# Optimization experiments

Measured on AMD Instinct MI355X. Metric: run time of the kernel, lower is better.

## Reference

```python
import jax, jax.numpy as jnp
from jax import lax
import numpy as np

B, S, V, H = 128, 1024, 128, 256


def setup_inputs() -> dict:
    key = jax.random.key(0)
    ks = jax.random.split(key, 12)
    sc = 1.0 / np.sqrt(H)
    return {
        "x": jax.random.normal(ks[0], (B, S, V), jnp.float32),
        "W_ih0": jax.random.normal(ks[1], (4 * H, V), jnp.float32) * sc,
        "W_hh0": jax.random.normal(ks[2], (4 * H, H), jnp.float32) * sc,
        "b_ih0": jax.random.normal(ks[3], (4 * H,), jnp.float32) * sc,
        "b_hh0": jax.random.normal(ks[4], (4 * H,), jnp.float32) * sc,
        "W_ih1": jax.random.normal(ks[5], (4 * H, H), jnp.float32) * sc,
        "W_hh1": jax.random.normal(ks[6], (4 * H, H), jnp.float32) * sc,
        "b_ih1": jax.random.normal(ks[7], (4 * H,), jnp.float32) * sc,
        "b_hh1": jax.random.normal(ks[8], (4 * H,), jnp.float32) * sc,
        "W_out": jax.random.normal(ks[9], (V, H), jnp.float32) * sc,
        "b_out": jax.random.normal(ks[10], (V,), jnp.float32) * sc,
    }


def _lstm_layer(x, W_ih, W_hh, b_ih, b_hh):
    # x: [B, S, in]; PyTorch gate order i, f, g, o along the 4H axis.
    b, s, _ = x.shape
    h_dim = W_hh.shape[1]
    # Precompute input contributions for all timesteps (one big GEMM).
    xg = jnp.einsum('bsi,gi->bsg', x, W_ih) + b_ih + b_hh  # [B, S, 4H]

    def step(carry, xg_t):
        h, c = carry
        g = xg_t + h @ W_hh.T  # [B, 4H]
        i, f, gg, o = jnp.split(g, 4, axis=-1)
        c = jax.nn.sigmoid(f) * c + jax.nn.sigmoid(i) * jnp.tanh(gg)
        h = jax.nn.sigmoid(o) * jnp.tanh(c)
        return (h, c), h

    h0 = jnp.zeros((b, h_dim), x.dtype)
    (_, _), hs = lax.scan(step, (h0, h0), jnp.swapaxes(xg, 0, 1))  # hs: [S, B, H]
    return jnp.swapaxes(hs, 0, 1)


def reference(x, W_ih0, W_hh0, b_ih0, b_hh0, W_ih1, W_hh1, b_ih1, b_hh1, W_out, b_out):
    h1 = _lstm_layer(x, W_ih0, W_hh0, b_ih0, b_hh0)
    h2 = _lstm_layer(h1, W_ih1, W_hh1, b_ih1, b_hh1)
    return jnp.einsum('bsh,vh->bsv', h2, W_out) + b_out
```

## Files before the change

kernel.cpp:

```cpp
#include <hip/hip_runtime.h>
#include <cstdint>

#define NB 128
#define NS 1024
#define NV 128
#define NH 256
#define CH 64
#define NCH (NS / CH)

typedef _Float16 f16;
typedef _Float16 h2 __attribute__((ext_vector_type(2)));
typedef _Float16 f16x8 __attribute__((ext_vector_type(8)));
typedef float f32x4 __attribute__((ext_vector_type(4)));
typedef uint32_t u32;

static __device__ __forceinline__ float fdot2(u32 a, u32 b, float c) {
  return __builtin_amdgcn_fdot2(__builtin_bit_cast(h2, a),
                                __builtin_bit_cast(h2, b), c, false);
}
static __device__ __forceinline__ u32 pkh(float a, float b) {
  union { h2 h; u32 u; } cv; cv.h = h2{(f16)a, (f16)b}; return cv.u;
}
static __device__ __forceinline__ u32 pkz(float a, float b) {
  return __builtin_bit_cast(u32, __builtin_amdgcn_cvt_pkrtz(a, b));
}
static __device__ __forceinline__ float sigm(float x) { return 1.f / (1.f + __expf(-x)); }
static __device__ __forceinline__ float tanh_(float x) { return 1.f - 2.f / (__expf(2.f * x) + 1.f); }

static __device__ __forceinline__ void pin4v(uint4& v) {
  asm volatile("" : "+v"(v.x), "+v"(v.y), "+v"(v.z), "+v"(v.w));
}

__global__ __launch_bounds__(1024) void prepack_kernel(
    const float* __restrict__ Wih0, const float* __restrict__ Wih1,
    const float* __restrict__ Whh0, const float* __restrict__ Whh1,
    u32* __restrict__ Wih0p, u32* __restrict__ Wih1p,
    u32* __restrict__ Whh0p, u32* __restrict__ Whh1p) {
  const int g = blockIdx.x * 1024 + threadIdx.x;
  const float* src; u32* dst; int off;
  if (g < 65536)       { src = Wih0; dst = Wih0p; off = g; }
  else if (g < 196608) { src = Wih1; dst = Wih1p; off = g - 65536; }
  else if (g < 327680) { src = Whh0; dst = Whh0p; off = g - 196608; }
  else                 { src = Whh1; dst = Whh1p; off = g - 327680; }
  dst[off] = pkh(src[2 * off], src[2 * off + 1]);
}

#define P1S 132
#define P0S 68
__global__ __launch_bounds__(512) void gemm_pair_kernel(
    const u32* __restrict__ g1_in, const u32* __restrict__ g1_Wp,
    const float* __restrict__ g1_bih, const float* __restrict__ g1_bhh,
    f16* __restrict__ g1_xg, int g1_t0, int g1_on,
    const float* __restrict__ g0_x, const u32* __restrict__ g0_Wp,
    const float* __restrict__ g0_bih, const float* __restrict__ g0_bhh,
    f16* __restrict__ g0_xg, int g0_t0, int g0_on) {
  __shared__ __align__(16) u32 panel[64 * P1S];
  const int tid = threadIdx.x;
  const int blk = blockIdx.x;
  const int lane = tid & 63;
  const int w = tid >> 6;
  const int lrow = lane & 15;
  const int lk = lane >> 4;

  if (blk < 128) {
    if (!g1_on) return;
    const int b = blk;
    {
      const uint4* src = (const uint4*)(g1_in + ((size_t)b * NS + g1_t0) * 128);
      const int t = tid >> 3, cc = tid & 7;
#pragma unroll
      for (int q = 0; q < 4; ++q) {
        uint4 v = src[t * 32 + cc * 4 + q];
        *(uint4*)&panel[t * P1S + cc * 16 + q * 4] = v;
      }
    }
    float bs[8];
#pragma unroll
    for (int n = 0; n < 8; ++n) {
      const int r = w * 128 + n * 16 + lrow;
      bs[n] = g1_bih[r] + g1_bhh[r];
    }
    __syncthreads();
    f32x4 acc[4][8] = {};
#pragma unroll 1
    for (int kc = 0; kc < 8; ++kc) {
      uint4 af[4];
#pragma unroll
      for (int m = 0; m < 4; ++m)
        af[m] = *(const uint4*)&panel[(m * 16 + lrow) * P1S + kc * 16 + lk * 4];
#pragma unroll
      for (int n = 0; n < 8; ++n) {
        const int r = w * 128 + n * 16 + lrow;
        uint4 bf = *(const uint4*)(g1_Wp + (size_t)r * 128 + kc * 16 + lk * 4);
#pragma unroll
        for (int m = 0; m < 4; ++m)
          acc[m][n] = __builtin_amdgcn_mfma_f32_16x16x32_f16(
              __builtin_bit_cast(f16x8, af[m]), __builtin_bit_cast(f16x8, bf),
              acc[m][n], 0, 0, 0);
      }
    }
#pragma unroll
    for (int m = 0; m < 4; ++m)
#pragma unroll
      for (int n = 0; n < 8; ++n) {
        const int r = w * 128 + n * 16 + lrow;
#pragma unroll
        for (int j = 0; j < 4; ++j) {
          const int t = m * 16 + lk * 4 + j;
          g1_xg[((size_t)b * CH + t) * 1024 + r] = (f16)(acc[m][n][j] + bs[n]);
        }
      }
  } else {
    if (!g0_on) return;
    const int b = blk - 128;
    {
      const float4* src = (const float4*)(g0_x + ((size_t)b * NS + g0_t0) * NV);
      const int t = tid >> 3, cc = tid & 7;
      float4 v0 = src[t * 32 + cc * 4 + 0];
      float4 v1 = src[t * 32 + cc * 4 + 1];
      float4 v2 = src[t * 32 + cc * 4 + 2];
      float4 v3 = src[t * 32 + cc * 4 + 3];
      *(uint4*)&panel[t * P0S + cc * 8 + 0] =
          uint4{pkz(v0.x, v0.y), pkz(v0.z, v0.w), pkz(v1.x, v1.y), pkz(v1.z, v1.w)};
      *(uint4*)&panel[t * P0S + cc * 8 + 4] =
          uint4{pkz(v2.x, v2.y), pkz(v2.z, v2.w), pkz(v3.x, v3.y), pkz(v3.z, v3.w)};
    }
    float bs[8];
#pragma unroll
    for (int n = 0; n < 8; ++n) {
      const int r = w * 128 + n * 16 + lrow;
      bs[n] = g0_bih[r] + g0_bhh[r];
    }
    __syncthreads();
    f32x4 acc[4][8] = {};
#pragma unroll 1
    for (int kc = 0; kc < 4; ++kc) {
      uint4 af[4];
#pragma unroll
      for (int m = 0; m < 4; ++m)
        af[m] = *(const uint4*)&panel[(m * 16 + lrow) * P0S + kc * 16 + lk * 4];
#pragma unroll
      for (int n = 0; n < 8; ++n) {
        const int r = w * 128 + n * 16 + lrow;
        uint4 bf = *(const uint4*)(g0_Wp + (size_t)r * 64 + kc * 16 + lk * 4);
#pragma unroll
        for (int m = 0; m < 4; ++m)
          acc[m][n] = __builtin_amdgcn_mfma_f32_16x16x32_f16(
              __builtin_bit_cast(f16x8, af[m]), __builtin_bit_cast(f16x8, bf),
              acc[m][n], 0, 0, 0);
      }
    }
#pragma unroll
    for (int m = 0; m < 4; ++m)
#pragma unroll
      for (int n = 0; n < 8; ++n) {
        const int r = w * 128 + n * 16 + lrow;
#pragma unroll
        for (int j = 0; j < 4; ++j) {
          const int t = m * 16 + lk * 4 + j;
          g0_xg[((size_t)b * CH + t) * 1024 + r] = (f16)(acc[m][n][j] + bs[n]);
        }
      }
  }
}

__global__ __attribute__((amdgpu_flat_work_group_size(1024, 1024),
                          amdgpu_waves_per_eu(4, 4)))
void scan_pair_kernel(
    const f16* __restrict__ xgA, const u32* __restrict__ WhhAp,
    u32* __restrict__ slotsA, u32* __restrict__ hseedA, float* __restrict__ carryA,
    int t0A, int firstA, int onA,
    const f16* __restrict__ xgB, const u32* __restrict__ WhhBp,
    u32* __restrict__ slotsB, u32* __restrict__ hseedB, float* __restrict__ carryB,
    int t0B, int firstB, int onB) {
  __shared__ uint4 wL0[4][1024];
  __shared__ uint4 wL1[4][1024];
  __shared__ __align__(16) u32 hbuf[2][128];

  const int blk = blockIdx.x;
  const int tid = threadIdx.x;
  const f16* xg; const u32* Whhp; u32* slots; u32* hseed; float* carry;
  int t0, first, b;
  if (blk < 128) {
    if (!onA) return;
    b = blk; xg = xgA; Whhp = WhhAp; slots = slotsA; hseed = hseedA; carry = carryA;
    t0 = t0A; first = firstA;
  } else {
    if (!onB) return;
    b = blk - 128; xg = xgB; Whhp = WhhBp; slots = slotsB; hseed = hseedB; carry = carryB;
    t0 = t0B; first = firstB;
  }
  const int kh = tid & 1;
  const int gp = (tid >> 1) & 1;
  const int u = tid >> 2;
  const int r0 = gp * 256 + u;
  const int r1 = r0 + 512;

  uint4 w0v[12], w1v[12];
  {
    const u32* p0 = Whhp + (size_t)r0 * 128 + kh * 64;
    const u32* p1 = Whhp + (size_t)r1 * 128 + kh * 64;
#pragma unroll
    for (int k = 0; k < 16; ++k) {
      uint4 v0 = *(const uint4*)(p0 + 4 * k);
      uint4 v1 = *(const uint4*)(p1 + 4 * k);
      if (k < 12) { w0v[k] = v0; w1v[k] = v1; }
      else { wL0[k - 12][tid] = v0; wL1[k - 12][tid] = v1; }
    }
  }
#pragma unroll
  for (int k = 0; k < 12; ++k) { pin4v(w0v[k]); pin4v(w1v[k]); }
  float c;
  if (first) {
    if (tid < 128) hbuf[0][tid] = 0u;
    c = 0.f;
  } else {
    if (tid < 128) hbuf[0][tid] = hseed[b * 128 + tid];
    c = carry[b * 256 + u];
  }
  __syncthreads();

#pragma unroll 1
  for (int tl = 0; tl < CH; ++tl) {
    const int cur = tl & 1, nxt = cur ^ 1;
    const f16* xp = xg + ((size_t)b * CH + tl) * 1024;
    const float xa = (float)xp[r0];
    const float xb = (float)xp[r1];

    float a0 = 0.f, a1 = 0.f;
#pragma unroll
    for (int k = 0; k < 16; ++k) {
      uint4 hk = *(const uint4*)&hbuf[cur][kh * 64 + 4 * k];
      const uint4 wa = (k < 12) ? w0v[k] : wL0[k - 12][tid];
      const uint4 wb = (k < 12) ? w1v[k] : wL1[k - 12][tid];
      a0 = fdot2(wa.x, hk.x, a0); a0 = fdot2(wa.y, hk.y, a0);
      a0 = fdot2(wa.z, hk.z, a0); a0 = fdot2(wa.w, hk.w, a0);
      a1 = fdot2(wb.x, hk.x, a1); a1 = fdot2(wb.y, hk.y, a1);
      a1 = fdot2(wb.z, hk.z, a1); a1 = fdot2(wb.w, hk.w, a1);
    }
    a0 += __shfl_xor(a0, 1);
    a1 += __shfl_xor(a1, 1);
    a0 += xa; a1 += xb;
    const float px0 = __shfl_xor(a0, 2);
    const float px1 = __shfl_xor(a1, 2);
    const float gi = sigm(gp ? px0 : a0);
    const float gf = sigm(gp ? a0 : px0);
    const float gg = tanh_(gp ? px1 : a1);
    const float go = sigm(gp ? a1 : px1);
    c = gf * c + gi * gg;
    const float h = go * tanh_(c);
    if ((tid & 3) == 0) {
      ((f16*)hbuf[nxt])[u] = (f16)h;
      ((f16*)(slots + ((size_t)b * NS + t0 + tl) * 128))[u] = (f16)h;
    }
    __syncthreads();
  }
  if (tid < 128) hseed[b * 128 + tid] = hbuf[0][tid];
  if ((tid & 3) == 0) carry[b * 256 + u] = c;
}

#define OPS 140
static __device__ __forceinline__ int swzc(int col) { return col + 4 * (col >> 5); }

__global__ __launch_bounds__(1024) void outproj_kernel(
    const float* __restrict__ Wout, const float* __restrict__ bout,
    u32* __restrict__ io) {
  const int bs = blockIdx.x;
  const int b = bs >> 4;
  const int t0 = (bs & 15) * 64;
  const int tid = threadIdx.x;
  const int p = tid & 7;
  const int vq = tid >> 3;

  __shared__ u32 h1L[64 * OPS];
  __shared__ float outL[64 * OPS];

  const u32* src = io + ((size_t)b * NS + t0) * 128;
  uint4 s0 = *(const uint4*)(src + (size_t)tid * 8);
  uint4 s1 = *(const uint4*)(src + (size_t)tid * 8 + 4);

  u32 wo[16];
  const float* pw = Wout + (size_t)vq * NH + p * 32;
#pragma unroll
  for (int k = 0; k < 8; ++k) {
    float4 w4 = *(const float4*)(pw + 4 * k);
    wo[2 * k] = pkh(w4.x, w4.y); wo[2 * k + 1] = pkh(w4.z, w4.w);
  }
  const float bo = bout[vq];

  {
    const int sr = tid >> 4;
    const int sc = (tid & 15) * 8;
    const int base = sr * OPS + swzc(sc);
    *(uint4*)&h1L[base] = s0;
    *(uint4*)&h1L[base + 4] = s1;
  }
  __syncthreads();

#pragma unroll 4
  for (int s = 0; s < 64; ++s) {
    float oa = 0.f;
#pragma unroll
    for (int q = 0; q < 4; ++q) {
      uint4 hq = *(const uint4*)&h1L[s * OPS + swzc(p * 16 + 4 * q)];
      u32 hw[4] = {hq.x, hq.y, hq.z, hq.w};
#pragma unroll
      for (int j = 0; j < 4; ++j) oa = fdot2(wo[4 * q + j], hw[j], oa);
    }
    oa += __shfl_xor(oa, 1);
    oa += __shfl_xor(oa, 2);
    oa += __shfl_xor(oa, 4);
    if (p == 0) outL[s * OPS + swzc(vq)] = oa + bo;
  }
  __syncthreads();

  float* df = (float*)(io + ((size_t)b * NS + t0) * 128);
  {
    const int sr = tid >> 4;
    const int sc = (tid & 15) * 8;
    const int base = sr * OPS + swzc(sc);
    *(float4*)(df + (size_t)tid * 8) = *(float4*)&outL[base];
    *(float4*)(df + (size_t)tid * 8 + 4) = *(float4*)&outL[base + 4];
  }
}

extern "C" void kernel_launch(void* const* d_in, const int* in_sizes, int n_in,
                              void* d_out, int out_size, void* d_ws, size_t ws_size,
                              hipStream_t stream) {
  const float* x    = (const float*)d_in[0];
  const float* Wih0 = (const float*)d_in[1];
  const float* Whh0 = (const float*)d_in[2];
  const float* bih0 = (const float*)d_in[3];
  const float* bhh0 = (const float*)d_in[4];
  const float* Wih1 = (const float*)d_in[5];
  const float* Whh1 = (const float*)d_in[6];
  const float* bih1 = (const float*)d_in[7];
  const float* bhh1 = (const float*)d_in[8];
  const float* Wout = (const float*)d_in[9];
  const float* bout = (const float*)d_in[10];

  f16* xg0 = (f16*)d_ws;
  f16* xg1 = (f16*)((char*)d_ws + (16u << 20));
  u32* hseed0 = (u32*)((char*)d_ws + (32u << 20));
  u32* hseed1 = (u32*)((char*)d_ws + (32u << 20) + (64u << 10));
  float* carry0 = (float*)((char*)d_ws + (32u << 20) + (128u << 10));
  float* carry1 = (float*)((char*)d_ws + (32u << 20) + (256u << 10));
  u32* Wih0p = (u32*)((char*)d_ws + (34u << 20));
  u32* Wih1p = (u32*)((char*)d_ws + (35u << 20));
  u32* Whh0p = (u32*)((char*)d_ws + (36u << 20));
  u32* Whh1p = (u32*)((char*)d_ws + (37u << 20));
  u32* slots = (u32*)d_out;

  prepack_kernel<<<448, 1024, 0, stream>>>(Wih0, Wih1, Whh0, Whh1,
                                           Wih0p, Wih1p, Whh0p, Whh1p);

  gemm_pair_kernel<<<256, 512, 0, stream>>>(
      nullptr, nullptr, nullptr, nullptr, nullptr, 0, 0,
      x, Wih0p, bih0, bhh0, xg0, 0, 1);
  scan_pair_kernel<<<256, 1024, 0, stream>>>(
      nullptr, nullptr, nullptr, nullptr, nullptr, 0, 0, 0,
      xg0, Whh0p, slots, hseed0, carry0, 0, 1, 1);

  for (int s = 0; s < NCH; ++s) {
    const int g0on = (s + 1 < NCH);
    gemm_pair_kernel<<<256, 512, 0, stream>>>(
        slots, Wih1p, bih1, bhh1, xg1, s * CH, 1,
        x, Wih0p, bih0, bhh0, xg0, (s + 1) * CH, g0on);
    scan_pair_kernel<<<256, 1024, 0, stream>>>(
        xg1, Whh1p, slots, hseed1, carry1, s * CH, (s == 0) ? 1 : 0, 1,
        xg0, Whh0p, slots, hseed0, carry0, (s + 1) * CH, 0, g0on);
  }
  outproj_kernel<<<2048, 1024, 0, stream>>>(Wout, bout, slots);
}
```

Before: 3.492 ms.

## Halve scan block to 512 threads with full-K rows per thread and readlane broadcast

The recurrent scan kernel drops from 1024 to 512 threads per block. Each thread now owns the whole K=256 reduction for two gate rows, so the cross-lane shuffle that combined K halves goes away. More of W_hh is kept in registers (24 of 32 uint4 chunks per row), with the remainder in LDS. The second half of the hidden vector is broadcast with readlane from a per-lane register copy instead of LDS reads, which cuts LDS traffic. The cost is twice the serial dot-product work per thread, much higher register pressure, and fewer waves to hide latency.

```diff
diff --git a/kernel.cpp b/kernel.cpp
--- a/kernel.cpp
+++ b/kernel.cpp
@@ -164,8 +164,8 @@
   }
 }
 
-__global__ __attribute__((amdgpu_flat_work_group_size(1024, 1024),
-                          amdgpu_waves_per_eu(4, 4)))
+__global__ __attribute__((amdgpu_flat_work_group_size(512, 512),
+                          amdgpu_waves_per_eu(2, 2)))
 void scan_pair_kernel(
     const f16* __restrict__ xgA, const u32* __restrict__ WhhAp,
     u32* __restrict__ slotsA, u32* __restrict__ hseedA, float* __restrict__ carryA,
@@ -173,8 +173,8 @@
     const f16* __restrict__ xgB, const u32* __restrict__ WhhBp,
     u32* __restrict__ slotsB, u32* __restrict__ hseedB, float* __restrict__ carryB,
     int t0B, int firstB, int onB) {
-  __shared__ uint4 wL0[4][1024];
-  __shared__ uint4 wL1[4][1024];
+  __shared__ uint4 wL0[8][512];
+  __shared__ uint4 wL1[8][512];
   __shared__ __align__(16) u32 hbuf[2][128];
 
   const int blk = blockIdx.x;
@@ -190,26 +190,26 @@
     b = blk - 128; xg = xgB; Whhp = WhhBp; slots = slotsB; hseed = hseedB; carry = carryB;
     t0 = t0B; first = firstB;
   }
-  const int kh = tid & 1;
-  const int gp = (tid >> 1) & 1;
-  const int u = tid >> 2;
-  const int r0 = gp * 256 + u;
+  const int p = tid & 1;
+  const int u = tid >> 1;
+  const int lane = tid & 63;
+  const int r0 = p * 256 + u;
   const int r1 = r0 + 512;
 
-  uint4 w0v[12], w1v[12];
+  uint4 w0r[24], w1r[24];
   {
-    const u32* p0 = Whhp + (size_t)r0 * 128 + kh * 64;
-    const u32* p1 = Whhp + (size_t)r1 * 128 + kh * 64;
-#pragma unroll
-    for (int k = 0; k < 16; ++k) {
+    const u32* p0 = Whhp + (size_t)r0 * 128;
+    const u32* p1 = Whhp + (size_t)r1 * 128;
+#pragma unroll
+    for (int k = 0; k < 32; ++k) {
       uint4 v0 = *(const uint4*)(p0 + 4 * k);
       uint4 v1 = *(const uint4*)(p1 + 4 * k);
-      if (k < 12) { w0v[k] = v0; w1v[k] = v1; }
-      else { wL0[k - 12][tid] = v0; wL1[k - 12][tid] = v1; }
-    }
-  }
-#pragma unroll
-  for (int k = 0; k < 12; ++k) { pin4v(w0v[k]); pin4v(w1v[k]); }
+      if (k < 24) { w0r[k] = v0; w1r[k] = v1; }
+      else { wL0[k - 24][tid] = v0; wL1[k - 24][tid] = v1; }
+    }
+  }
+#pragma unroll
+  for (int k = 0; k < 24; ++k) { pin4v(w0r[k]); pin4v(w1r[k]); }
   float c;
   if (first) {
     if (tid < 128) hbuf[0][tid] = 0u;
@@ -227,36 +227,50 @@
     const float xa = (float)xp[r0];
     const float xb = (float)xp[r1];
 
+    const uint2 hv = *(const uint2*)&hbuf[cur][2 * lane];
+
     float a0 = 0.f, a1 = 0.f;
 #pragma unroll
     for (int k = 0; k < 16; ++k) {
-      uint4 hk = *(const uint4*)&hbuf[cur][kh * 64 + 4 * k];
-      const uint4 wa = (k < 12) ? w0v[k] : wL0[k - 12][tid];
-      const uint4 wb = (k < 12) ? w1v[k] : wL1[k - 12][tid];
+      uint4 hk = *(const uint4*)&hbuf[cur][4 * k];
+      const uint4 wa = w0r[k];
+      const uint4 wb = w1r[k];
       a0 = fdot2(wa.x, hk.x, a0); a0 = fdot2(wa.y, hk.y, a0);
       a0 = fdot2(wa.z, hk.z, a0); a0 = fdot2(wa.w, hk.w, a0);
       a1 = fdot2(wb.x, hk.x, a1); a1 = fdot2(wb.y, hk.y, a1);
       a1 = fdot2(wb.z, hk.z, a1); a1 = fdot2(wb.w, hk.w, a1);
     }
-    a0 += __shfl_xor(a0, 1);
-    a1 += __shfl_xor(a1, 1);
+#pragma unroll
+    for (int k = 16; k < 32; ++k) {
+      const u32 s0 = (u32)__builtin_amdgcn_readlane((int)hv.x, 2 * k);
+      const u32 s1 = (u32)__builtin_amdgcn_readlane((int)hv.y, 2 * k);
+      const u32 s2 = (u32)__builtin_amdgcn_readlane((int)hv.x, 2 * k + 1);
+      const u32 s3 = (u32)__builtin_amdgcn_readlane((int)hv.y, 2 * k + 1);
+      const uint4 wa = (k < 24) ? w0r[k] : wL0[k - 24][tid];
+      const uint4 wb = (k < 24) ? w1r[k] : wL1[k - 24][tid];
+      a0 = fdot2(wa.x, s0, a0); a0 = fdot2(wa.y, s1, a0);
+      a0 = fdot2(wa.z, s2, a0); a0 = fdot2(wa.w, s3, a0);
+      a1 = fdot2(wb.x, s0, a1); a1 = fdot2(wb.y, s1, a1);
+      a1 = fdot2(wb.z, s2, a1); a1 = fdot2(wb.w, s3, a1);
+    }
     a0 += xa; a1 += xb;
-    const float px0 = __shfl_xor(a0, 2);
-    const float px1 = __shfl_xor(a1, 2);
-    const float gi = sigm(gp ? px0 : a0);
-    const float gf = sigm(gp ? a0 : px0);
-    const float gg = tanh_(gp ? px1 : a1);
-    const float go = sigm(gp ? a1 : px1);
+    const float px0 = __shfl_xor(a0, 1);
+    const float px1 = __shfl_xor(a1, 1);
+    const float ai = p ? px0 : a0;
+    const float ag = p ? px1 : a1;
+    const float af = p ? a0 : px0;
+    const float ao = p ? a1 : px1;
+    const float gi = sigm(ai), gg = tanh_(ag), gf = sigm(af), go = sigm(ao);
     c = gf * c + gi * gg;
     const float h = go * tanh_(c);
-    if ((tid & 3) == 0) {
+    if (p == 0) {
       ((f16*)hbuf[nxt])[u] = (f16)h;
       ((f16*)(slots + ((size_t)b * NS + t0 + tl) * 128))[u] = (f16)h;
     }
     __syncthreads();
   }
   if (tid < 128) hseed[b * 128 + tid] = hbuf[0][tid];
-  if ((tid & 3) == 0) carry[b * 256 + u] = c;
+  if (p == 0) carry[b * 256 + u] = c;
 }
 
 #define OPS 140
@@ -357,7 +371,7 @@
   gemm_pair_kernel<<<256, 512, 0, stream>>>(
       nullptr, nullptr, nullptr, nullptr, nullptr, 0, 0,
       x, Wih0p, bih0, bhh0, xg0, 0, 1);
-  scan_pair_kernel<<<256, 1024, 0, stream>>>(
+  scan_pair_kernel<<<256, 512, 0, stream>>>(
       nullptr, nullptr, nullptr, nullptr, nullptr, 0, 0, 0,
       xg0, Whh0p, slots, hseed0, carry0, 0, 1, 1);
 
@@ -366,7 +380,7 @@
     gemm_pair_kernel<<<256, 512, 0, stream>>>(
         slots, Wih1p, bih1, bhh1, xg1, s * CH, 1,
         x, Wih0p, bih0, bhh0, xg0, (s + 1) * CH, g0on);
-    scan_pair_kernel<<<256, 1024, 0, stream>>>(
+    scan_pair_kernel<<<256, 512, 0, stream>>>(
         xg1, Whh1p, slots, hseed1, carry1, s * CH, (s == 0) ? 1 : 0, 1,
         xg0, Whh0p, slots, hseed0, carry0, (s + 1) * CH, 0, g0on);
   }
```

Result: faster. 3.191 ms, median of 2 (-8.6%).

## Rewrite LSTM scan as 16-batch MFMA recurrence with AGPR-resident weights

Applied to the files above, without the earlier changes.

The recurrent step is recast from per-batch fdot2 dot products (256 blocks of 1024 threads, one batch row each) into 16x16x32 MFMA tiles. Each 512-thread block now handles 16 batch rows, and its W_hh slice is held in accumulator registers. The xg input for the next timestep is prefetched into double-buffered LDS, and the h stores to global memory are deferred by one step. This cuts ALU work per step and amortises the weights over 16 batches. In exchange, only 16 blocks run in parallel, so most CUs sit idle and each step is bound by MFMA latency.

```diff
diff --git a/kernel.cpp b/kernel.cpp
--- a/kernel.cpp
+++ b/kernel.cpp
@@ -27,8 +27,8 @@
 static __device__ __forceinline__ float sigm(float x) { return 1.f / (1.f + __expf(-x)); }
 static __device__ __forceinline__ float tanh_(float x) { return 1.f - 2.f / (__expf(2.f * x) + 1.f); }
 
-static __device__ __forceinline__ void pin4v(uint4& v) {
-  asm volatile("" : "+v"(v.x), "+v"(v.y), "+v"(v.z), "+v"(v.w));
+static __device__ __forceinline__ void pin4a(uint4& v) {
+  asm volatile("" : "+a"(v.x), "+a"(v.y), "+a"(v.z), "+a"(v.w));
 }
 
 __global__ __launch_bounds__(1024) void prepack_kernel(
@@ -164,8 +164,10 @@
   }
 }
 
-__global__ __attribute__((amdgpu_flat_work_group_size(1024, 1024),
-                          amdgpu_waves_per_eu(4, 4)))
+#define HLS 132
+#define XGS 1032
+__global__ __attribute__((amdgpu_flat_work_group_size(512, 512),
+                          amdgpu_waves_per_eu(2, 2)))
 void scan_pair_kernel(
     const f16* __restrict__ xgA, const u32* __restrict__ WhhAp,
     u32* __restrict__ slotsA, u32* __restrict__ hseedA, float* __restrict__ carryA,
@@ -173,90 +175,148 @@
     const f16* __restrict__ xgB, const u32* __restrict__ WhhBp,
     u32* __restrict__ slotsB, u32* __restrict__ hseedB, float* __restrict__ carryB,
     int t0B, int firstB, int onB) {
-  __shared__ uint4 wL0[4][1024];
-  __shared__ uint4 wL1[4][1024];
-  __shared__ __align__(16) u32 hbuf[2][128];
-
+  __shared__ __align__(16) u32 hL[2][16 * HLS];
+  __shared__ __align__(16) f16 xgs[2][16 * XGS];
   const int blk = blockIdx.x;
   const int tid = threadIdx.x;
-  const f16* xg; const u32* Whhp; u32* slots; u32* hseed; float* carry;
-  int t0, first, b;
-  if (blk < 128) {
+  const f16* xg; const u32* Wp; u32* slots; u32* hseed; float* carry;
+  int t0, first, bg;
+  if (blk < 8) {
     if (!onA) return;
-    b = blk; xg = xgA; Whhp = WhhAp; slots = slotsA; hseed = hseedA; carry = carryA;
+    bg = blk; xg = xgA; Wp = WhhAp; slots = slotsA; hseed = hseedA; carry = carryA;
     t0 = t0A; first = firstA;
   } else {
     if (!onB) return;
-    b = blk - 128; xg = xgB; Whhp = WhhBp; slots = slotsB; hseed = hseedB; carry = carryB;
+    bg = blk - 8; xg = xgB; Wp = WhhBp; slots = slotsB; hseed = hseedB; carry = carryB;
     t0 = t0B; first = firstB;
   }
-  const int kh = tid & 1;
-  const int gp = (tid >> 1) & 1;
-  const int u = tid >> 2;
-  const int r0 = gp * 256 + u;
-  const int r1 = r0 + 512;
-
-  uint4 w0v[12], w1v[12];
+  const int lane = tid & 63;
+  const int w = tid >> 6;
+  const int lrow = lane & 15;
+  const int lk = lane >> 4;
+  const int m_ = tid >> 5;
+  const int c4 = tid & 31;
+
+  uint4 wB[64];
+#pragma unroll
+  for (int s = 0; s < 2; ++s)
+#pragma unroll
+    for (int g = 0; g < 4; ++g) {
+      const int r = g * 256 + (w + 8 * s) * 16 + lrow;
+      const u32* pr = Wp + (size_t)r * 128 + lk * 4;
+#pragma unroll
+      for (int kc = 0; kc < 8; ++kc)
+        wB[(s * 4 + g) * 8 + kc] = *(const uint4*)(pr + kc * 16);
+    }
+#pragma unroll
+  for (int k = 0; k < 64; ++k) pin4a(wB[k]);
+
+  if (first) {
+    *(uint4*)&hL[0][m_ * HLS + c4 * 4] = uint4{0u, 0u, 0u, 0u};
+  } else {
+    *(uint4*)&hL[0][m_ * HLS + c4 * 4] =
+        *(const uint4*)(hseed + (size_t)(bg * 16 + m_) * 128 + c4 * 4);
+  }
   {
-    const u32* p0 = Whhp + (size_t)r0 * 128 + kh * 64;
-    const u32* p1 = Whhp + (size_t)r1 * 128 + kh * 64;
-#pragma unroll
-    for (int k = 0; k < 16; ++k) {
-      uint4 v0 = *(const uint4*)(p0 + 4 * k);
-      uint4 v1 = *(const uint4*)(p1 + 4 * k);
-      if (k < 12) { w0v[k] = v0; w1v[k] = v1; }
-      else { wL0[k - 12][tid] = v0; wL1[k - 12][tid] = v1; }
-    }
-  }
-#pragma unroll
-  for (int k = 0; k < 12; ++k) { pin4v(w0v[k]); pin4v(w1v[k]); }
-  float c;
+    const f16* sp = xg + ((size_t)(bg * 16 + m_) * CH + 0) * 1024 + c4 * 32;
+    f16* dp = &xgs[0][m_ * XGS + c4 * 32];
+    *(uint4*)(dp + 0)  = *(const uint4*)(sp + 0);
+    *(uint4*)(dp + 8)  = *(const uint4*)(sp + 8);
+    *(uint4*)(dp + 16) = *(const uint4*)(sp + 16);
+    *(uint4*)(dp + 24) = *(const uint4*)(sp + 24);
+  }
+  float cst[2][4], hpv[2][4];
   if (first) {
-    if (tid < 128) hbuf[0][tid] = 0u;
-    c = 0.f;
+#pragma unroll
+    for (int s = 0; s < 2; ++s)
+#pragma unroll
+      for (int j = 0; j < 4; ++j) cst[s][j] = 0.f;
   } else {
-    if (tid < 128) hbuf[0][tid] = hseed[b * 128 + tid];
-    c = carry[b * 256 + u];
+#pragma unroll
+    for (int s = 0; s < 2; ++s) {
+      const int u = (w + 8 * s) * 16 + lrow;
+#pragma unroll
+      for (int j = 0; j < 4; ++j)
+        cst[s][j] = carry[(size_t)(bg * 16 + lk * 4 + j) * 256 + u];
+    }
   }
   __syncthreads();
 
 #pragma unroll 1
   for (int tl = 0; tl < CH; ++tl) {
     const int cur = tl & 1, nxt = cur ^ 1;
-    const f16* xp = xg + ((size_t)b * CH + tl) * 1024;
-    const float xa = (float)xp[r0];
-    const float xb = (float)xp[r1];
-
-    float a0 = 0.f, a1 = 0.f;
-#pragma unroll
-    for (int k = 0; k < 16; ++k) {
-      uint4 hk = *(const uint4*)&hbuf[cur][kh * 64 + 4 * k];
-      const uint4 wa = (k < 12) ? w0v[k] : wL0[k - 12][tid];
-      const uint4 wb = (k < 12) ? w1v[k] : wL1[k - 12][tid];
-      a0 = fdot2(wa.x, hk.x, a0); a0 = fdot2(wa.y, hk.y, a0);
-      a0 = fdot2(wa.z, hk.z, a0); a0 = fdot2(wa.w, hk.w, a0);
-      a1 = fdot2(wb.x, hk.x, a1); a1 = fdot2(wb.y, hk.y, a1);
-      a1 = fdot2(wb.z, hk.z, a1); a1 = fdot2(wb.w, hk.w, a1);
-    }
-    a0 += __shfl_xor(a0, 1);
-    a1 += __shfl_xor(a1, 1);
-    a0 += xa; a1 += xb;
-    const float px0 = __shfl_xor(a0, 2);
-    const float px1 = __shfl_xor(a1, 2);
-    const float gi = sigm(gp ? px0 : a0);
-    const float gf = sigm(gp ? a0 : px0);
-    const float gg = tanh_(gp ? px1 : a1);
-    const float go = sigm(gp ? a1 : px1);
-    c = gf * c + gi * gg;
-    const float h = go * tanh_(c);
-    if ((tid & 3) == 0) {
-      ((f16*)hbuf[nxt])[u] = (f16)h;
-      ((f16*)(slots + ((size_t)b * NS + t0 + tl) * 128))[u] = (f16)h;
+    if (tl > 0) {
+#pragma unroll
+      for (int s = 0; s < 2; ++s) {
+        const int u = (w + 8 * s) * 16 + lrow;
+#pragma unroll
+        for (int j = 0; j < 4; ++j)
+          ((f16*)slots)[((size_t)(bg * 16 + lk * 4 + j) * NS + (t0 + tl - 1)) * 256 + u] =
+              (f16)hpv[s][j];
+      }
+    }
+    uint4 pf0, pf1, pf2, pf3;
+    {
+      const int tn = (tl + 1 < CH) ? tl + 1 : tl;
+      const f16* sp = xg + ((size_t)(bg * 16 + m_) * CH + tn) * 1024 + c4 * 32;
+      pf0 = *(const uint4*)(sp + 0);
+      pf1 = *(const uint4*)(sp + 8);
+      pf2 = *(const uint4*)(sp + 16);
+      pf3 = *(const uint4*)(sp + 24);
+    }
+    uint4 af[8];
+#pragma unroll
+    for (int kc = 0; kc < 8; ++kc)
+      af[kc] = *(const uint4*)&hL[cur][lrow * HLS + kc * 16 + lk * 4];
+    f32x4 acc[8] = {};
+#pragma unroll
+    for (int kc = 0; kc < 8; ++kc)
+#pragma unroll
+      for (int q = 0; q < 8; ++q)
+        acc[q] = __builtin_amdgcn_mfma_f32_16x16x32_f16(
+            __builtin_bit_cast(f16x8, af[kc]), __builtin_bit_cast(f16x8, wB[q * 8 + kc]),
+            acc[q], 0, 0, 0);
+#pragma unroll
+    for (int s = 0; s < 2; ++s) {
+      const int ub = (w + 8 * s) * 16 + lrow;
+#pragma unroll
+      for (int j = 0; j < 4; ++j) {
+        const int m = lk * 4 + j;
+        const float xi = (float)xgs[cur][m * XGS + 0   + ub];
+        const float xf = (float)xgs[cur][m * XGS + 256 + ub];
+        const float xc = (float)xgs[cur][m * XGS + 512 + ub];
+        const float xo = (float)xgs[cur][m * XGS + 768 + ub];
+        const float gi = sigm(acc[s * 4 + 0][j] + xi);
+        const float gf = sigm(acc[s * 4 + 1][j] + xf);
+        const float gg = tanh_(acc[s * 4 + 2][j] + xc);
+        const float go = sigm(acc[s * 4 + 3][j] + xo);
+        cst[s][j] = gf * cst[s][j] + gi * gg;
+        const float h = go * tanh_(cst[s][j]);
+        hpv[s][j] = h;
+        ((f16*)&hL[nxt][0])[m * (HLS * 2) + ub] = (f16)h;
+      }
+    }
+    {
+      f16* dp = &xgs[nxt][m_ * XGS + c4 * 32];
+      *(uint4*)(dp + 0)  = pf0;
+      *(uint4*)(dp + 8)  = pf1;
+      *(uint4*)(dp + 16) = pf2;
+      *(uint4*)(dp + 24) = pf3;
     }
     __syncthreads();
   }
-  if (tid < 128) hseed[b * 128 + tid] = hbuf[0][tid];
-  if ((tid & 3) == 0) carry[b * 256 + u] = c;
+#pragma unroll
+  for (int s = 0; s < 2; ++s) {
+    const int u = (w + 8 * s) * 16 + lrow;
+#pragma unroll
+    for (int j = 0; j < 4; ++j) {
+      ((f16*)slots)[((size_t)(bg * 16 + lk * 4 + j) * NS + (t0 + CH - 1)) * 256 + u] =
+          (f16)hpv[s][j];
+      carry[(size_t)(bg * 16 + lk * 4 + j) * 256 + u] = cst[s][j];
+    }
+  }
+  *(uint4*)(hseed + (size_t)(bg * 16 + m_) * 128 + c4 * 4) =
+      *(const uint4*)&hL[0][m_ * HLS + c4 * 4];
 }
 
 #define OPS 140
@@ -357,7 +417,7 @@
   gemm_pair_kernel<<<256, 512, 0, stream>>>(
       nullptr, nullptr, nullptr, nullptr, nullptr, 0, 0,
       x, Wih0p, bih0, bhh0, xg0, 0, 1);
-  scan_pair_kernel<<<256, 1024, 0, stream>>>(
+  scan_pair_kernel<<<16, 512, 0, stream>>>(
       nullptr, nullptr, nullptr, nullptr, nullptr, 0, 0, 0,
       xg0, Whh0p, slots, hseed0, carry0, 0, 1, 1);
 
@@ -366,7 +426,7 @@
     gemm_pair_kernel<<<256, 512, 0, stream>>>(
         slots, Wih1p, bih1, bhh1, xg1, s * CH, 1,
         x, Wih0p, bih0, bhh0, xg0, (s + 1) * CH, g0on);
-    scan_pair_kernel<<<256, 1024, 0, stream>>>(
+    scan_pair_kernel<<<16, 512, 0, stream>>>(
         xg1, Whh1p, slots, hseed1, carry1, s * CH, (s == 0) ? 1 : 0, 1,
         xg0, Whh0p, slots, hseed0, carry0, (s + 1) * CH, 0, g0on);
   }
```

Result: slower. 13.04 ms (+273.5%).
